# Kernel tuning notes

Measured on AMD Instinct MI355X. Metric: run time of the kernel, lower is better.

The kernel has to match this reference:

```python
import jax, jax.numpy as jnp
import numpy as np

B, S, D = 2, 2048, 512
P, T, MAP_H = 13, 5, 64


def setup_inputs() -> dict:
    key = jax.random.key(0)
    ks = jax.random.split(key, 8)
    s = 0.02
    return {
        "hidden_states": jax.random.normal(ks[0], (B, S, D), jnp.float32),
        "ln_gamma": jnp.ones((D,), jnp.float32),
        "ln_beta": jnp.zeros((D,), jnp.float32),
        "W_in": jax.random.normal(ks[1], (D, P * D), jnp.float32) * s,
        "b_in": jnp.zeros((P * D,), jnp.float32),
        "W_map1": jax.random.normal(ks[2], (D, MAP_H), jnp.float32) * s,
        "b_map1": jnp.zeros((MAP_H,), jnp.float32),
        "W_map2": jax.random.normal(ks[3], (MAP_H, T), jnp.float32) * s,
        "b_map2": jnp.zeros((T,), jnp.float32),
        "log_tau": jnp.linspace(0.0, 4.0, T).astype(jnp.float32),
        "mix": jax.random.normal(ks[4], (P, T), jnp.float32) / float(P * T),
        "W_out": jax.random.normal(ks[5], (D, D), jnp.float32) * s,
        "b_out": jnp.zeros((D,), jnp.float32),
        "scale": jnp.float32(1e-3),
        "h_prev": jnp.zeros((B, P, T, D), jnp.float32),
        "position_offset": 0,
    }


def _forward(hidden_states, ln_gamma, ln_beta, W_in, b_in, W_map1, b_map1,
             W_map2, b_map2, log_tau, mix, W_out, b_out, scale, h_prev):
    b, s_len, d = hidden_states.shape
    p, t = mix.shape
    # pre-norm (LayerNorm, eps=1e-5)
    mu = jnp.mean(hidden_states, -1, keepdims=True)
    var = jnp.var(hidden_states, -1, keepdims=True)
    xn = (hidden_states - mu) * jax.lax.rsqrt(var + 1e-5) * ln_gamma + ln_beta
    # per-protofilament input drive: [B,S,P,D]
    u = (xn @ W_in + b_in).reshape(b, s_len, p, d)
    # liquid (input-dependent) decay per time scale: [B,S,T]
    gate = jax.nn.sigmoid(jnp.tanh(xn @ W_map1 + b_map1) @ W_map2 + b_map2)
    alpha = jnp.exp(-gate / jnp.exp(log_tau))  # [B,S,T]

    def step(h, inp):
        u_t, a_t = inp                      # [B,P,D], [B,T]
        a = a_t[:, None, :, None]           # broadcast over P and D
        h = a * h + (1.0 - a) * u_t[:, :, None, :]   # [B,P,T,D]
        y = jnp.einsum('bptd,pt->bd', h, mix)        # mix protofilaments/time scales
        return h, y

    _, ys = jax.lax.scan(step, h_prev,
                         (jnp.moveaxis(u, 1, 0), jnp.moveaxis(alpha, 1, 0)))
    mt_out = jnp.moveaxis(ys, 0, 1) @ W_out + b_out  # [B,S,D]
    return hidden_states + scale * mt_out


def reference(hidden_states, ln_gamma, ln_beta, W_in, b_in, W_map1, b_map1,
              W_map2, b_map2, log_tau, mix, W_out, b_out, scale, h_prev,
              position_offset):
    return _forward(hidden_states, ln_gamma, ln_beta, W_in, b_in, W_map1,
                    b_map1, W_map2, b_map2, log_tau, mix, W_out, b_out,
                    scale, h_prev)
```

## Files before the change

### kernel.cpp

```cpp
#include <hip/hip_runtime.h>
#include <hip/hip_bf16.h>
#include <stdint.h>

#define BB 2
#define SS 2048
#define DD 512
#define PP 13
#define TT 5
#define MH 64
#define MM (BB*SS)
#define NV (TT*DD)
#define KK 512
#define CHUNK 16
#define NCH (SS/CHUNK)

typedef __attribute__((ext_vector_type(4))) float f32x4;
typedef __attribute__((ext_vector_type(8))) short s8v;
typedef unsigned int u32;
typedef __attribute__((address_space(3))) u32 lds_u32_t;
typedef __attribute__((address_space(1))) const u32 glb_u32_t;

__device__ __forceinline__ float bf2f(unsigned short u){
  union { unsigned int i; float f; } c; c.i = ((unsigned int)u) << 16; return c.f;
}
__device__ __forceinline__ unsigned short f2bf(float f){
  union { float f; unsigned int i; } c; c.f = f;
  unsigned int x = c.i;
  unsigned int r = (x + 0x7fffu + ((x >> 16) & 1u)) >> 16;
  return (unsigned short)r;
}
__device__ __forceinline__ void gld16(unsigned short* l, const unsigned short* g){
  __builtin_amdgcn_global_load_lds((glb_u32_t*)g, (lds_u32_t*)l, 16, 0, 0);
}

__global__ __launch_bounds__(256) void k_prep_ln(
    const float* __restrict__ hs,
    const float* __restrict__ gamma, const float* __restrict__ beta,
    const float* __restrict__ W_in, const float* __restrict__ b_in,
    const float* __restrict__ mix,  const float* __restrict__ W_out,
    const float* __restrict__ W1,   const float* __restrict__ b1,
    const float* __restrict__ W2,   const float* __restrict__ b2,
    const float* __restrict__ ltau,
    unsigned short* __restrict__ xn_bf,
    unsigned short* __restrict__ W_vT, float* __restrict__ b_v,
    unsigned short* __restrict__ W_outT,
    float* __restrict__ alpha)
{
  __shared__ unsigned short W1L[MH][KK];
  int blk = blockIdx.x;
  if (blk < 64){
    int gb = blk;
    int tid = threadIdx.x, lane = tid & 63, w = tid >> 6;
    int lr = lane & 15, kq = lane >> 4;
    int row = gb*64 + w*16 + lr;
    #pragma unroll 4
    for (int i=0;i<128;++i){
      int idx = i*256 + tid;
      int n = idx & 63, k = idx >> 6;
      int slot = (k >> 3) ^ (n & 7);
      W1L[n][slot*8 + (k & 7)] = f2bf(W1[idx]);
    }
    float v[16][8];
    float s = 0.f, sq = 0.f;
    const float* xr = hs + (size_t)row*DD + kq*8;
    #pragma unroll
    for (int kt=0;kt<16;++kt){
      float4 a0 = *(const float4*)(xr + kt*32);
      float4 a1 = *(const float4*)(xr + kt*32 + 4);
      v[kt][0]=a0.x; v[kt][1]=a0.y; v[kt][2]=a0.z; v[kt][3]=a0.w;
      v[kt][4]=a1.x; v[kt][5]=a1.y; v[kt][6]=a1.z; v[kt][7]=a1.w;
      s  += a0.x+a0.y+a0.z+a0.w + a1.x+a1.y+a1.z+a1.w;
      sq += a0.x*a0.x+a0.y*a0.y+a0.z*a0.z+a0.w*a0.w
          + a1.x*a1.x+a1.y*a1.y+a1.z*a1.z+a1.w*a1.w;
    }
    s  += __shfl_xor(s,16);  s  += __shfl_xor(s,32);
    sq += __shfl_xor(sq,16); sq += __shfl_xor(sq,32);
    float mu   = s  * (1.f/DD);
    float var  = sq * (1.f/DD) - mu*mu;
    float rstd = rsqrtf(var + 1e-5f);
    s8v af[16];
    #pragma unroll
    for (int kt=0;kt<16;++kt){
      float4 g0 = *(const float4*)(gamma + kq*8 + kt*32);
      float4 g1 = *(const float4*)(gamma + kq*8 + kt*32 + 4);
      float4 t0 = *(const float4*)(beta  + kq*8 + kt*32);
      float4 t1 = *(const float4*)(beta  + kq*8 + kt*32 + 4);
      union { unsigned short us[8]; s8v v8; } o;
      o.us[0] = f2bf((v[kt][0]-mu)*rstd*g0.x + t0.x);
      o.us[1] = f2bf((v[kt][1]-mu)*rstd*g0.y + t0.y);
      o.us[2] = f2bf((v[kt][2]-mu)*rstd*g0.z + t0.z);
      o.us[3] = f2bf((v[kt][3]-mu)*rstd*g0.w + t0.w);
      o.us[4] = f2bf((v[kt][4]-mu)*rstd*g1.x + t1.x);
      o.us[5] = f2bf((v[kt][5]-mu)*rstd*g1.y + t1.y);
      o.us[6] = f2bf((v[kt][6]-mu)*rstd*g1.z + t1.z);
      o.us[7] = f2bf((v[kt][7]-mu)*rstd*g1.w + t1.w);
      af[kt] = o.v8;
    }
    __syncthreads();
    f32x4 acc[4];
    #pragma unroll
    for (int ni=0;ni<4;++ni) acc[ni] = (f32x4){0.f,0.f,0.f,0.f};
    #pragma unroll
    for (int kt=0;kt<16;++kt){
      #pragma unroll
      for (int ni=0;ni<4;++ni){
        int n = ni*16 + lr;
        int slot = (kt*4 + kq) ^ (n & 7);
        union { uint4 u; s8v v8; } bfr;
        bfr.u = *(const uint4*)&W1L[n][slot*8];
        acc[ni] = __builtin_amdgcn_mfma_f32_16x16x32_bf16(af[kt], bfr.v8, acc[ni], 0,0,0);
      }
    }
    float z1[4][4];
    #pragma unroll
    for (int ni=0;ni<4;++ni){
      float bb = b1[ni*16+lr];
      #pragma unroll
      for (int r=0;r<4;++r) z1[r][ni] = tanhf(acc[ni][r] + bb);
    }
    float et[TT];
    #pragma unroll
    for (int t=0;t<TT;++t) et[t] = expf(-ltau[t]);
    float av[4][TT];
    #pragma unroll
    for (int t=0;t<TT;++t){
      float w2v[4];
      #pragma unroll
      for (int ni=0;ni<4;++ni) w2v[ni] = W2[(ni*16+lr)*TT + t];
      #pragma unroll
      for (int r=0;r<4;++r){
        float p = z1[r][0]*w2v[0] + z1[r][1]*w2v[1] + z1[r][2]*w2v[2] + z1[r][3]*w2v[3];
        #pragma unroll
        for (int o=8;o>0;o>>=1) p += __shfl_xor(p, o);
        float z2 = p + b2[t];
        float gate = 1.f/(1.f + expf(-z2));
        av[r][t] = expf(-gate * et[t]);
      }
    }
    if (lr < TT){
      int t = lr;
      #pragma unroll
      for (int r=0;r<4;++r){
        int orow = gb*64 + w*16 + kq*4 + r;
        alpha[(size_t)orow*TT + t] = av[r][t];
      }
    }
  } else if (blk < 1088){
    int tid = threadIdx.x;
    int lane = tid & 63;
    int row = (blk-64)*4 + (tid>>6);
    const float* x = hs + (size_t)row*DD + lane*8;
    float4 v0 = *(const float4*)x;
    float4 v1 = *(const float4*)(x+4);
    float s  = v0.x+v0.y+v0.z+v0.w + v1.x+v1.y+v1.z+v1.w;
    float sq = v0.x*v0.x+v0.y*v0.y+v0.z*v0.z+v0.w*v0.w
             + v1.x*v1.x+v1.y*v1.y+v1.z*v1.z+v1.w*v1.w;
    #pragma unroll
    for (int o=32;o>0;o>>=1){ s += __shfl_xor(s,o); sq += __shfl_xor(sq,o); }
    float mu   = s  * (1.f/DD);
    float var  = sq * (1.f/DD) - mu*mu;
    float rstd = rsqrtf(var + 1e-5f);
    float4 g0 = *(const float4*)(gamma + lane*8);
    float4 g1 = *(const float4*)(gamma + lane*8 + 4);
    float4 b0 = *(const float4*)(beta  + lane*8);
    float4 b1v = *(const float4*)(beta + lane*8 + 4);
    union { unsigned short us[8]; uint4 u; } pk;
    pk.us[0] = f2bf((v0.x-mu)*rstd*g0.x + b0.x);
    pk.us[1] = f2bf((v0.y-mu)*rstd*g0.y + b0.y);
    pk.us[2] = f2bf((v0.z-mu)*rstd*g0.z + b0.z);
    pk.us[3] = f2bf((v0.w-mu)*rstd*g0.w + b0.w);
    pk.us[4] = f2bf((v1.x-mu)*rstd*g1.x + b1v.x);
    pk.us[5] = f2bf((v1.y-mu)*rstd*g1.y + b1v.y);
    pk.us[6] = f2bf((v1.z-mu)*rstd*g1.z + b1v.z);
    pk.us[7] = f2bf((v1.w-mu)*rstd*g1.w + b1v.w);
    *(uint4*)(xn_bf + (size_t)row*DD + lane*8) = pk.u;
  } else if (blk < 1216){
    int idx = (blk-1088) * 256 + threadIdx.x;
    int d  = idx & (DD-1);
    int k0 = idx >> 9;
    float mx[PP][TT];
    #pragma unroll
    for (int p=0;p<PP;++p)
      #pragma unroll
      for (int t=0;t<TT;++t) mx[p][t] = mix[p*TT+t];
    float acc[TT][8];
    #pragma unroll
    for (int t=0;t<TT;++t)
      #pragma unroll
      for (int j=0;j<8;++j) acc[t][j] = 0.f;
    #pragma unroll
    for (int j=0;j<8;++j){
      int k = k0*8 + j;
      const float* wrow = W_in + (size_t)k * (PP*DD) + d;
      #pragma unroll
      for (int p=0;p<PP;++p){
        float w = wrow[p*DD];
        #pragma unroll
        for (int t=0;t<TT;++t) acc[t][j] += mx[p][t]*w;
      }
    }
    #pragma unroll
    for (int t=0;t<TT;++t){
      union { unsigned short us[8]; uint4 u; } pk;
      #pragma unroll
      for (int j=0;j<8;++j) pk.us[j] = f2bf(acc[t][j]);
      *(uint4*)(W_vT + ((size_t)(t*DD+d))*KK + k0*8) = pk.u;
    }
    if (k0 == 0){
      #pragma unroll
      for (int t=0;t<TT;++t){
        float s = 0.f;
        #pragma unroll
        for (int p=0;p<PP;++p) s += mx[p][t]*b_in[p*DD+d];
        b_v[t*DD+d] = s;
      }
    }
  } else {
    int idx = (blk-1216)*256 + threadIdx.x;
    int n  = idx & (DD-1);
    int k0 = idx >> 9;
    union { unsigned short us[8]; uint4 u; } pk;
    #pragma unroll
    for (int j=0;j<8;++j) pk.us[j] = f2bf(W_out[(size_t)(k0*8+j)*DD + n]);
    *(uint4*)(W_outT + (size_t)n*KK + k0*8) = pk.u;
  }
}

template<int BN, int NDIM, bool OUTEPI>
__global__ __launch_bounds__(256, 4) void k_gemm(
    const unsigned short* __restrict__ A,
    const unsigned short* __restrict__ Bt,
    const float* __restrict__ bias,
    const float* __restrict__ hidden,
    const float* __restrict__ scale_p,
    float* __restrict__ outF,
    unsigned short* __restrict__ outBf)
{
  constexpr int NI  = (BN == 128) ? 4 : 2;
  constexpr int WNT = BN / 2;
  constexpr int NLD = (BN == 128) ? 4 : 3;
  __shared__ unsigned short lA[2][128*32];
  __shared__ unsigned short lB[2][BN*32];
  int bid = blockIdx.y * gridDim.x + blockIdx.x;
  int nwg = gridDim.x * gridDim.y;
  int swz = (bid & 7) * (nwg >> 3) + (bid >> 3);
  int bn = swz % gridDim.x, bm = swz / gridDim.x;
  int tid  = threadIdx.x;
  int lane = tid & 63;
  int w    = tid >> 6;
  int wm = w >> 1, wn = w & 1;
  f32x4 acc[4][NI];
  #pragma unroll
  for (int i=0;i<4;++i)
    #pragma unroll
    for (int j=0;j<NI;++j) acc[i][j] = (f32x4){0.f,0.f,0.f,0.f};

  int srow  = lane >> 2;
  int slotS = (lane & 3) ^ (srow & 3);
  const uint8_t* gA = (const uint8_t*)(A + (size_t)(bm*128 + w*32 + srow)*KK) + slotS*16;
  const uint8_t* gB;
  if constexpr (BN == 128) gB = (const uint8_t*)(Bt + (size_t)(bn*BN + w*32 + srow)*KK) + slotS*16;
  else                     gB = (const uint8_t*)(Bt + (size_t)(bn*BN + w*16 + srow)*KK) + slotS*16;
  int lr = lane & 15, kq = lane >> 4;
  int kqs = kq ^ (lr & 3);

  auto stage = [&](int buf, int kt){
    int off = kt*64;
    gld16(&lA[buf][(w*32)*32],    (const unsigned short*)(gA + off));
    gld16(&lA[buf][(w*32+16)*32], (const unsigned short*)(gA + (size_t)16*KK*2 + off));
    if constexpr (BN == 128){
      gld16(&lB[buf][(w*32)*32],    (const unsigned short*)(gB + off));
      gld16(&lB[buf][(w*32+16)*32], (const unsigned short*)(gB + (size_t)16*KK*2 + off));
    } else {
      gld16(&lB[buf][(w*16)*32],    (const unsigned short*)(gB + off));
    }
  };
  auto compute = [&](int buf){
    union { uint4 u; s8v v; } af[4], bfr[NI];
    #pragma unroll
    for (int mi=0;mi<4;++mi) af[mi].u  = *(const uint4*)&lA[buf][(wm*64+mi*16+lr)*32 + kqs*8];
    #pragma unroll
    for (int ni=0;ni<NI;++ni) bfr[ni].u = *(const uint4*)&lB[buf][(wn*WNT+ni*16+lr)*32 + kqs*8];
    #pragma unroll
    for (int mi=0;mi<4;++mi)
      #pragma unroll
      for (int ni=0;ni<NI;++ni)
        acc[mi][ni] = __builtin_amdgcn_mfma_f32_16x16x32_bf16(af[mi].v, bfr[ni].v, acc[mi][ni], 0,0,0);
  };

  stage(0, 0);
  #pragma unroll
  for (int kt=0; kt<16; ++kt){
    if (kt < 15){
      stage((kt+1)&1, kt+1);
      if constexpr (NLD == 4) asm volatile("s_waitcnt vmcnt(4)" ::: "memory");
      else                    asm volatile("s_waitcnt vmcnt(3)" ::: "memory");
    } else {
      asm volatile("s_waitcnt vmcnt(0)" ::: "memory");
    }
    __builtin_amdgcn_sched_barrier(0);
    __builtin_amdgcn_s_barrier();
    __builtin_amdgcn_sched_barrier(0);
    compute(kt&1);
    __builtin_amdgcn_sched_barrier(0);
    __builtin_amdgcn_s_barrier();
  }

  float sc = 0.f;
  if constexpr (OUTEPI) sc = *scale_p;
  #pragma unroll
  for (int mi=0;mi<4;++mi){
    #pragma unroll
    for (int ni=0;ni<NI;++ni){
      int row = bm*128 + wm*64 + mi*16 + kq*4;
      int col = bn*BN  + wn*WNT + ni*16 + lr;
      float bs = bias[col];
      f32x4 c = acc[mi][ni];
      #pragma unroll
      for (int r=0;r<4;++r){
        float val = c[r] + bs;
        size_t off = (size_t)(row+r)*NDIM + col;
        if constexpr (OUTEPI) outF[off] = hidden[off] + sc*val;
        else                  outBf[off] = f2bf(val);
      }
    }
  }
}

__global__ __launch_bounds__(320) void k_scan_a(
    const float* __restrict__ alpha,
    const unsigned short* __restrict__ v,
    float* __restrict__ L, float* __restrict__ PA,
    unsigned short* __restrict__ yloc)
{
  int blk = blockIdx.x;
  int c = blk & (NCH-1), b = blk >> 7;
  int tid = threadIdx.x;
  int t  = tid >> 6;
  int d8 = tid & 63;
  __shared__ float sAl[CHUNK*TT];
  __shared__ unsigned short yl[TT][8][DD];
  if (tid < CHUNK*TT) sAl[tid] = alpha[(size_t)(b*SS + c*CHUNK)*TT + tid];
  __syncthreads();
  const unsigned short* vp = v + (size_t)(b*SS + c*CHUNK)*NV + t*DD + d8*8;
  float g[8];
  #pragma unroll
  for (int j=0;j<8;++j) g[j] = 0.f;
  float pa = 1.f;
  #pragma unroll
  for (int half=0; half<2; ++half){
    uint4 vv[8];
    #pragma unroll
    for (int s=0;s<8;++s) vv[s] = *(const uint4*)(vp + (size_t)(half*8+s)*NV);
    #pragma unroll
    for (int s=0;s<8;++s){
      float a = sAl[(half*8+s)*TT+t], om = 1.f - a;
      const unsigned short* pv = (const unsigned short*)&vv[s];
      union { unsigned short us[8]; uint4 u; } o;
      #pragma unroll
      for (int j=0;j<8;++j){ g[j] = a*g[j] + om*bf2f(pv[j]); o.us[j] = f2bf(g[j]); }
      *(uint4*)&yl[t][s][d8*8] = o.u;
      pa *= a;
    }
    __syncthreads();
    if (t < 4){
      #pragma unroll
      for (int ii=0; ii<2; ++ii){
        int s = t*2 + ii;
        float y[8];
        #pragma unroll
        for (int j=0;j<8;++j) y[j] = 0.f;
        #pragma unroll
        for (int tt=0;tt<TT;++tt){
          uint4 gv = *(const uint4*)&yl[tt][s][d8*8];
          const unsigned short* gp = (const unsigned short*)&gv;
          #pragma unroll
          for (int j=0;j<8;++j) y[j] += bf2f(gp[j]);
        }
        union { unsigned short us[8]; uint4 u; } o;
        #pragma unroll
        for (int j=0;j<8;++j) o.us[j] = f2bf(y[j]);
        *(uint4*)(yloc + (size_t)(b*SS + c*CHUNK + half*8 + s)*DD + d8*8) = o.u;
      }
    }
    __syncthreads();
  }
  float* Lp = L + ((size_t)(b*TT+t)*NCH + c)*DD + d8*8;
  *(float4*)Lp     = (float4){g[0],g[1],g[2],g[3]};
  *(float4*)(Lp+4) = (float4){g[4],g[5],g[6],g[7]};
  if (d8 == 0) PA[(size_t)(b*TT+t)*NCH + c] = pa;
}

__global__ __launch_bounds__(512) void k_scan_b(
    const float* __restrict__ mix,
    const float* __restrict__ h_prev,
    const float* __restrict__ PA,
    const float* __restrict__ L,
    float* __restrict__ Gc)
{
  int blk = blockIdx.x;
  int t = blk % TT, b = blk / TT;
  int d = threadIdx.x;
  __shared__ float sP[NCH];
  if (d < NCH) sP[d] = PA[(size_t)(b*TT+t)*NCH + d];
  __syncthreads();
  float carry = 0.f;
  #pragma unroll
  for (int p=0;p<PP;++p)
    carry += mix[p*TT+t] * h_prev[((size_t)(b*PP+p)*TT + t)*DD + d];
  const float* Lp = L  + (size_t)(b*TT+t)*NCH*DD + d;
  float*       gc = Gc + (size_t)(b*TT+t)*NCH*DD + d;
  float buf[8], nbuf[8];
  #pragma unroll
  for (int j=0;j<8;++j) buf[j] = Lp[(size_t)j*DD];
  for (int c0=0;c0<NCH;c0+=8){
    if (c0+8 < NCH){
      #pragma unroll
      for (int j=0;j<8;++j) nbuf[j] = Lp[(size_t)(c0+8+j)*DD];
    }
    #pragma unroll
    for (int j=0;j<8;++j){
      gc[(size_t)(c0+j)*DD] = carry;
      carry = sP[c0+j]*carry + buf[j];
    }
    #pragma unroll
    for (int j=0;j<8;++j) buf[j] = nbuf[j];
  }
}

__global__ __launch_bounds__(256) void k_scan_c(
    const float* __restrict__ alpha,
    const unsigned short* __restrict__ yloc,
    const float* __restrict__ Gc,
    unsigned short* __restrict__ ybf)
{
  int blk = blockIdx.x;
  int c = blk & (NCH-1), b = blk >> 7;
  int tid = threadIdx.x;
  int s4 = tid >> 6;
  int d8 = tid & 63;
  __shared__ float sAl[CHUNK*TT];
  if (tid < CHUNK*TT) sAl[tid] = alpha[(size_t)(b*SS + c*CHUNK)*TT + tid];
  __syncthreads();
  float ca[TT][8];
  #pragma unroll
  for (int t=0;t<TT;++t){
    const float* gp = Gc + ((size_t)(b*TT+t)*NCH + c)*DD + d8*8;
    float4 c0 = *(const float4*)gp;
    float4 c1 = *(const float4*)(gp+4);
    ca[t][0]=c0.x; ca[t][1]=c0.y; ca[t][2]=c0.z; ca[t][3]=c0.w;
    ca[t][4]=c1.x; ca[t][5]=c1.y; ca[t][6]=c1.z; ca[t][7]=c1.w;
  }
  float pr[TT];
  #pragma unroll
  for (int t=0;t<TT;++t){
    float p = 1.f;
    for (int j=0;j<s4*4;++j) p *= sAl[j*TT+t];
    pr[t] = p;
  }
  const unsigned short* yp = yloc + (size_t)(b*SS + c*CHUNK)*DD + d8*8;
  unsigned short* op = ybf + (size_t)(b*SS + c*CHUNK)*DD + d8*8;
  #pragma unroll
  for (int i=0;i<4;++i){
    int s2 = s4*4 + i;
    uint4 yv = *(const uint4*)(yp + (size_t)s2*DD);
    const unsigned short* yq = (const unsigned short*)&yv;
    float y[8];
    #pragma unroll
    for (int j=0;j<8;++j) y[j] = bf2f(yq[j]);
    #pragma unroll
    for (int t=0;t<TT;++t){
      pr[t] *= sAl[s2*TT+t];
      #pragma unroll
      for (int j=0;j<8;++j) y[j] += pr[t]*ca[t][j];
    }
    union { unsigned short us[8]; uint4 u; } o;
    #pragma unroll
    for (int j=0;j<8;++j) o.us[j] = f2bf(y[j]);
    *(uint4*)(op + (size_t)s2*DD) = o.u;
  }
}

extern "C" void kernel_launch(void* const* d_in, const int* in_sizes, int n_in,
                              void* d_out, int out_size, void* d_ws, size_t ws_size,
                              hipStream_t stream)
{
  (void)in_sizes; (void)n_in; (void)out_size; (void)ws_size;
  const float* hs     = (const float*)d_in[0];
  const float* gamma  = (const float*)d_in[1];
  const float* beta   = (const float*)d_in[2];
  const float* W_in   = (const float*)d_in[3];
  const float* b_in   = (const float*)d_in[4];
  const float* W1     = (const float*)d_in[5];
  const float* b1     = (const float*)d_in[6];
  const float* W2     = (const float*)d_in[7];
  const float* b2     = (const float*)d_in[8];
  const float* ltau   = (const float*)d_in[9];
  const float* mix    = (const float*)d_in[10];
  const float* W_out  = (const float*)d_in[11];
  const float* b_out  = (const float*)d_in[12];
  const float* scale  = (const float*)d_in[13];
  const float* h_prev = (const float*)d_in[14];
  float* out = (float*)d_out;

  uint8_t* w = (uint8_t*)d_ws;
  unsigned short* xn   = (unsigned short*)(w);
  unsigned short* WvT  = (unsigned short*)(w + 4194304);
  unsigned short* WoT  = (unsigned short*)(w + 6815744);
  float* alphaB        = (float*)(w + 7340032);
  float* b_v           = (float*)(w + 7421952);
  float* PA            = (float*)(w + 7432192);
  float* L             = (float*)(w + 7437312);
  float* Gc            = (float*)(w + 10058752);
  unsigned short* vg   = (unsigned short*)(w + 12680192);
  unsigned short* ybf  = (unsigned short*)(w + 33651712);
  unsigned short* yloc = xn;

  hipLaunchKernelGGL(k_prep_ln, dim3(1344), dim3(256), 0, stream,
                     hs, gamma, beta, W_in, b_in, mix, W_out, W1, b1, W2, b2, ltau,
                     xn, WvT, b_v, WoT, alphaB);
  hipLaunchKernelGGL((k_gemm<128,NV,false>), dim3(NV/128, MM/128), dim3(256), 0, stream,
                     xn, WvT, b_v, nullptr, nullptr, nullptr, vg);
  hipLaunchKernelGGL(k_scan_a, dim3(BB*NCH), dim3(320), 0, stream, alphaB, vg, L, PA, yloc);
  hipLaunchKernelGGL(k_scan_b, dim3(BB*TT), dim3(512), 0, stream, mix, h_prev, PA, L, Gc);
  hipLaunchKernelGGL(k_scan_c, dim3(BB*NCH), dim3(256), 0, stream, alphaB, yloc, Gc, ybf);
  hipLaunchKernelGGL((k_gemm<64,DD,true>), dim3(DD/64, MM/128), dim3(256), 0, stream,
                     ybf, WoT, b_out, hs, scale, out, nullptr);
}
```

Measured before the change: 76.86 us.

## Store scan carries in bf16, split scan_b across more blocks, halve W1 LDS

The chunk-local sums L and the carry-in values Gc are now stored in bf16 instead of fp32, which halves the traffic between the three scan kernels. The sequential cross-chunk scan kernel now launches twice as many 256-thread blocks and prefetches 16 chunks at a time instead of 8, giving a little more parallelism on its serial critical path. The prep kernel stages W1 into LDS in two 256-row halves, cutting shared memory per block, perhaps to allow more resident blocks. Storing the carries in bf16 adds rounding error to the scan state.

```diff
diff --git a/kernel.cpp b/kernel.cpp
--- a/kernel.cpp
+++ b/kernel.cpp
@@ -46,20 +46,13 @@
     unsigned short* __restrict__ W_outT,
     float* __restrict__ alpha)
 {
-  __shared__ unsigned short W1L[MH][KK];
+  __shared__ unsigned short W1L[MH][256];
   int blk = blockIdx.x;
   if (blk < 64){
     int gb = blk;
     int tid = threadIdx.x, lane = tid & 63, w = tid >> 6;
     int lr = lane & 15, kq = lane >> 4;
     int row = gb*64 + w*16 + lr;
-    #pragma unroll 4
-    for (int i=0;i<128;++i){
-      int idx = i*256 + tid;
-      int n = idx & 63, k = idx >> 6;
-      int slot = (k >> 3) ^ (n & 7);
-      W1L[n][slot*8 + (k & 7)] = f2bf(W1[idx]);
-    }
     float v[16][8];
     float s = 0.f, sq = 0.f;
     const float* xr = hs + (size_t)row*DD + kq*8;
@@ -96,19 +89,30 @@
       o.us[7] = f2bf((v[kt][7]-mu)*rstd*g1.w + t1.w);
       af[kt] = o.v8;
     }
-    __syncthreads();
     f32x4 acc[4];
     #pragma unroll
     for (int ni=0;ni<4;++ni) acc[ni] = (f32x4){0.f,0.f,0.f,0.f};
     #pragma unroll
-    for (int kt=0;kt<16;++kt){
-      #pragma unroll
-      for (int ni=0;ni<4;++ni){
-        int n = ni*16 + lr;
-        int slot = (kt*4 + kq) ^ (n & 7);
-        union { uint4 u; s8v v8; } bfr;
-        bfr.u = *(const uint4*)&W1L[n][slot*8];
-        acc[ni] = __builtin_amdgcn_mfma_f32_16x16x32_bf16(af[kt], bfr.v8, acc[ni], 0,0,0);
+    for (int half=0; half<2; ++half){
+      __syncthreads();
+      #pragma unroll 4
+      for (int i=0;i<64;++i){
+        int idx = i*256 + tid;
+        int n = idx & 63, kl = idx >> 6;
+        int slot = (kl >> 3) ^ (n & 7);
+        W1L[n][slot*8 + (kl & 7)] = f2bf(W1[(size_t)(half*256 + kl)*MH + n]);
+      }
+      __syncthreads();
+      #pragma unroll
+      for (int ktl=0;ktl<8;++ktl){
+        #pragma unroll
+        for (int ni=0;ni<4;++ni){
+          int n = ni*16 + lr;
+          int slot = (ktl*4 + kq) ^ (n & 7);
+          union { uint4 u; s8v v8; } bfr;
+          bfr.u = *(const uint4*)&W1L[n][slot*8];
+          acc[ni] = __builtin_amdgcn_mfma_f32_16x16x32_bf16(af[half*8+ktl], bfr.v8, acc[ni], 0,0,0);
+        }
       }
     }
     float z1[4][4];
@@ -330,7 +334,7 @@
 __global__ __launch_bounds__(320) void k_scan_a(
     const float* __restrict__ alpha,
     const unsigned short* __restrict__ v,
-    float* __restrict__ L, float* __restrict__ PA,
+    unsigned short* __restrict__ L, float* __restrict__ PA,
     unsigned short* __restrict__ yloc)
 {
   int blk = blockIdx.x;
@@ -385,53 +389,55 @@
     }
     __syncthreads();
   }
-  float* Lp = L + ((size_t)(b*TT+t)*NCH + c)*DD + d8*8;
-  *(float4*)Lp     = (float4){g[0],g[1],g[2],g[3]};
-  *(float4*)(Lp+4) = (float4){g[4],g[5],g[6],g[7]};
+  union { unsigned short us[8]; uint4 u; } lo;
+  #pragma unroll
+  for (int j=0;j<8;++j) lo.us[j] = f2bf(g[j]);
+  *(uint4*)(L + ((size_t)(b*TT+t)*NCH + c)*DD + d8*8) = lo.u;
   if (d8 == 0) PA[(size_t)(b*TT+t)*NCH + c] = pa;
 }
 
-__global__ __launch_bounds__(512) void k_scan_b(
+__global__ __launch_bounds__(256) void k_scan_b(
     const float* __restrict__ mix,
     const float* __restrict__ h_prev,
     const float* __restrict__ PA,
-    const float* __restrict__ L,
-    float* __restrict__ Gc)
+    const unsigned short* __restrict__ L,
+    unsigned short* __restrict__ Gc)
 {
   int blk = blockIdx.x;
-  int t = blk % TT, b = blk / TT;
-  int d = threadIdx.x;
+  int bt = blk >> 1;
+  int t = bt % TT, b = bt / TT;
+  int d = (blk & 1)*256 + threadIdx.x;
   __shared__ float sP[NCH];
-  if (d < NCH) sP[d] = PA[(size_t)(b*TT+t)*NCH + d];
+  if (threadIdx.x < NCH) sP[threadIdx.x] = PA[(size_t)bt*NCH + threadIdx.x];
   __syncthreads();
   float carry = 0.f;
   #pragma unroll
   for (int p=0;p<PP;++p)
     carry += mix[p*TT+t] * h_prev[((size_t)(b*PP+p)*TT + t)*DD + d];
-  const float* Lp = L  + (size_t)(b*TT+t)*NCH*DD + d;
-  float*       gc = Gc + (size_t)(b*TT+t)*NCH*DD + d;
-  float buf[8], nbuf[8];
-  #pragma unroll
-  for (int j=0;j<8;++j) buf[j] = Lp[(size_t)j*DD];
-  for (int c0=0;c0<NCH;c0+=8){
-    if (c0+8 < NCH){
-      #pragma unroll
-      for (int j=0;j<8;++j) nbuf[j] = Lp[(size_t)(c0+8+j)*DD];
-    }
-    #pragma unroll
-    for (int j=0;j<8;++j){
-      gc[(size_t)(c0+j)*DD] = carry;
+  const unsigned short* Lp = L  + (size_t)bt*NCH*DD + d;
+  unsigned short*       gc = Gc + (size_t)bt*NCH*DD + d;
+  float buf[16], nbuf[16];
+  #pragma unroll
+  for (int j=0;j<16;++j) buf[j] = bf2f(Lp[(size_t)j*DD]);
+  for (int c0=0;c0<NCH;c0+=16){
+    if (c0+16 < NCH){
+      #pragma unroll
+      for (int j=0;j<16;++j) nbuf[j] = bf2f(Lp[(size_t)(c0+16+j)*DD]);
+    }
+    #pragma unroll
+    for (int j=0;j<16;++j){
+      gc[(size_t)(c0+j)*DD] = f2bf(carry);
       carry = sP[c0+j]*carry + buf[j];
     }
     #pragma unroll
-    for (int j=0;j<8;++j) buf[j] = nbuf[j];
+    for (int j=0;j<16;++j) buf[j] = nbuf[j];
   }
 }
 
 __global__ __launch_bounds__(256) void k_scan_c(
     const float* __restrict__ alpha,
     const unsigned short* __restrict__ yloc,
-    const float* __restrict__ Gc,
+    const unsigned short* __restrict__ Gc,
     unsigned short* __restrict__ ybf)
 {
   int blk = blockIdx.x;
@@ -445,11 +451,10 @@
   float ca[TT][8];
   #pragma unroll
   for (int t=0;t<TT;++t){
-    const float* gp = Gc + ((size_t)(b*TT+t)*NCH + c)*DD + d8*8;
-    float4 c0 = *(const float4*)gp;
-    float4 c1 = *(const float4*)(gp+4);
-    ca[t][0]=c0.x; ca[t][1]=c0.y; ca[t][2]=c0.z; ca[t][3]=c0.w;
-    ca[t][4]=c1.x; ca[t][5]=c1.y; ca[t][6]=c1.z; ca[t][7]=c1.w;
+    uint4 gv = *(const uint4*)(Gc + ((size_t)(b*TT+t)*NCH + c)*DD + d8*8);
+    const unsigned short* gp = (const unsigned short*)&gv;
+    #pragma unroll
+    for (int j=0;j<8;++j) ca[t][j] = bf2f(gp[j]);
   }
   float pr[TT];
   #pragma unroll
@@ -510,8 +515,8 @@
   float* alphaB        = (float*)(w + 7340032);
   float* b_v           = (float*)(w + 7421952);
   float* PA            = (float*)(w + 7432192);
-  float* L             = (float*)(w + 7437312);
-  float* Gc            = (float*)(w + 10058752);
+  unsigned short* L    = (unsigned short*)(w + 7437312);
+  unsigned short* Gc   = (unsigned short*)(w + 10058752);
   unsigned short* vg   = (unsigned short*)(w + 12680192);
   unsigned short* ybf  = (unsigned short*)(w + 33651712);
   unsigned short* yloc = xn;
@@ -522,7 +527,7 @@
   hipLaunchKernelGGL((k_gemm<128,NV,false>), dim3(NV/128, MM/128), dim3(256), 0, stream,
                      xn, WvT, b_v, nullptr, nullptr, nullptr, vg);
   hipLaunchKernelGGL(k_scan_a, dim3(BB*NCH), dim3(320), 0, stream, alphaB, vg, L, PA, yloc);
-  hipLaunchKernelGGL(k_scan_b, dim3(BB*TT), dim3(512), 0, stream, mix, h_prev, PA, L, Gc);
+  hipLaunchKernelGGL(k_scan_b, dim3(2*BB*TT), dim3(256), 0, stream, mix, h_prev, PA, L, Gc);
   hipLaunchKernelGGL(k_scan_c, dim3(BB*NCH), dim3(256), 0, stream, alphaB, yloc, Gc, ybf);
   hipLaunchKernelGGL((k_gemm<64,DD,true>), dim3(DD/64, MM/128), dim3(256), 0, stream,
                      ybf, WoT, b_out, hs, scale, out, nullptr);
```

Result: slower. 84.81 us (+10.3%).
